# Performance work log

Hardware: AMD Instinct MI355X
Metric: run time of the kernel (lower is better)

The kernel has to match this reference:

```python
import jax, jax.numpy as jnp
import numpy as np

L = 2        # rnn_num_layer
H = 512      # rnn_hidden_size
E = 512      # embed_dim == rnn_input_size
B = 16
T_DEC = 512
S_ENC = 512
VOCAB = 1001 # num_embed
OUT = 1000   # output_size
PAD = 0.0


def setup_inputs() -> dict:
    key = jax.random.key(0)
    ks = jax.random.split(key, 16)
    s = 0.05
    trg_inputs = jax.random.randint(ks[0], (B, T_DEC), 0, VOCAB)
    trg_len = jnp.clip(jax.random.randint(ks[1], (B,), 0, T_DEC + 1), 1, T_DEC)
    encoder_outputs = jax.random.normal(ks[2], (B, S_ENC, H), dtype=jnp.float32)
    h0 = jax.random.normal(ks[3], (L * 2, B, H), dtype=jnp.float32)
    c0 = jax.random.normal(ks[4], (L * 2, B, H), dtype=jnp.float32)
    embed = jax.random.normal(ks[5], (VOCAB, E)) * s
    W_ih0 = jax.random.normal(ks[6], (2, 4 * H, E)) * s          # layer 0, fwd/bwd dirs
    W_ih1 = jax.random.normal(ks[7], (L - 1, 2, 4 * H, 2 * H)) * s  # layers>0 take concat(fwd,bwd)
    W_hh = jax.random.normal(ks[8], (L, 2, 4 * H, H)) * s
    b_ih = jax.random.normal(ks[9], (L, 2, 4 * H)) * s
    b_hh = jax.random.normal(ks[10], (L, 2, 4 * H)) * s
    W_att = jax.random.normal(ks[11], (H, H)) * s  # Attention 'general' linear
    b_att = jax.random.normal(ks[12], (H,)) * s
    W_fc = jax.random.normal(ks[13], (OUT, 2 * H)) * s
    b_fc = jax.random.normal(ks[14], (OUT,)) * s
    return dict(trg_inputs=trg_inputs, trg_len=trg_len, encoder_outputs=encoder_outputs,
                h0=h0, c0=c0, embed=embed, W_ih0=W_ih0, W_ih1=W_ih1, W_hh=W_hh,
                b_ih=b_ih, b_hh=b_hh, W_att=W_att, b_att=b_att, W_fc=W_fc, b_fc=b_fc)


def _cell(x, h, c, Wi, Wh, bi, bh):
    # PyTorch LSTM gate order: i, f, g, o
    g = x @ Wi.T + h @ Wh.T + bi + bh  # [B, 4H]
    i, f, gg, o = jnp.split(g, 4, axis=-1)
    c2 = jax.nn.sigmoid(f) * c + jax.nn.sigmoid(i) * jnp.tanh(gg)
    h2 = jax.nn.sigmoid(o) * jnp.tanh(c2)
    return h2, c2


def _decode(trg_inputs, trg_len, encoder_outputs, h0, c0, embed,
            W_ih0, W_ih1, W_hh, b_ih, b_hh, W_att, b_att, W_fc, b_fc):
    Bb, T = trg_inputs.shape
    S = encoder_outputs.shape[1]
    # 'general' attention projection of encoder outputs (hoisted out of the loop)
    enc_proj = jnp.einsum('bsh,gh->bsg', encoder_outputs, W_att) + b_att
    enc_mask = jnp.arange(S)[None, :] < trg_len[:, None]          # [B, S]
    step_valid = jnp.arange(T)[:, None] < trg_len[None, :]        # [T, B]
    h = h0.reshape(L, 2, Bb, H)
    c = c0.reshape(L, 2, Bb, H)

    def step(carry, xt):
        h, c = carry
        tok, valid = xt                                           # [B], [B]
        xin = embed[tok]                                          # [B, E]
        hs, cs = [], []
        for l in range(L):
            Wi = W_ih0 if l == 0 else W_ih1[l - 1]
            hf, cf = _cell(xin, h[l, 0], c[l, 0], Wi[0], W_hh[l, 0], b_ih[l, 0], b_hh[l, 0])
            hb, cb = _cell(xin, h[l, 1], c[l, 1], Wi[1], W_hh[l, 1], b_ih[l, 1], b_hh[l, 1])
            hs.append(jnp.stack([hf, hb]))
            cs.append(jnp.stack([cf, cb]))
            xin = jnp.concatenate([hf, hb], axis=-1)              # input to next layer [B, 2H]
        h2 = jnp.stack(hs)
        c2 = jnp.stack(cs)
        dec = hs[-1][0] + hs[-1][1]                               # sum fwd+bwd halves [B, H]
        score = jnp.einsum('bh,bsh->bs', dec, enc_proj)
        score = jnp.where(enc_mask, score, -1e30)                 # ragged length mask
        att = jax.nn.softmax(score, axis=-1)
        ctx = jnp.einsum('bs,bsh->bh', att, encoder_outputs)
        fc = jnp.concatenate([dec, ctx], axis=-1) @ W_fc.T + b_fc # [B, OUT]
        out = jnp.where(valid[:, None], fc, PAD)                  # positions past trg_len stay pad
        return (h2, c2), out

    _, outs = jax.lax.scan(step, (h, c), (trg_inputs.T, step_valid))
    return outs.transpose(1, 0, 2)                                # [B, T, OUT]


def reference(trg_inputs, trg_len, encoder_outputs, h0, c0, embed,
              W_ih0, W_ih1, W_hh, b_ih, b_hh, W_att, b_att, W_fc, b_fc):
    return _decode(trg_inputs, trg_len, encoder_outputs, h0, c0, embed,
                   W_ih0, W_ih1, W_hh, b_ih, b_hh, W_att, b_att, W_fc, b_fc)
```

## Files before the change

kernel.cpp:

```cpp
#include <hip/hip_runtime.h>
#include <cstdint>
#include <cstddef>

typedef __attribute__((ext_vector_type(8))) short short8;
typedef __attribute__((ext_vector_type(4))) float f32x4;
typedef __attribute__((ext_vector_type(4))) unsigned int uint4v;

#define DEV static __device__ __forceinline__

DEV float b2f(unsigned short u){ union{unsigned int i; float f;} v; v.i = ((unsigned int)u)<<16; return v.f; }
DEV unsigned short f2b(float f){
  union{float f; unsigned int i;} v; v.f = f;
  unsigned int u = v.i;
  unsigned int r = (u + 0x7fffu + ((u>>16)&1u)) >> 16;
  return (unsigned short)r;
}
DEV float sigm(float x){ return 1.0f/(1.0f + __expf(-x)); }
DEV float tanhfast(float x){ return 1.0f - 2.0f/(1.0f + __expf(2.0f*x)); }

DEV uint4v ld_sc_b128(const unsigned short* p){
  uint4v d;
  asm volatile("global_load_dwordx4 %0, %1, off sc0 sc1" : "=v"(d) : "v"(p) : "memory");
  return d;
}
DEV short8 ldw8(const float* p){
  short8 w;
  #pragma unroll
  for (int e = 0; e < 8; ++e) w[e] = (short)f2b(p[e]);
  return w;
}

__global__ __launch_bounds__(256) void k_cast(const float* __restrict__ s, unsigned short* __restrict__ d, int n){
  int i = blockIdx.x*256 + threadIdx.x;
  if (i < n) d[i] = f2b(s[i]);
}
__global__ __launch_bounds__(256) void k_transpose_enc(const float* __restrict__ enc, unsigned short* __restrict__ encT){
  int i = blockIdx.x*256 + threadIdx.x;
  if (i >= 16*512*512) return;
  int b = i >> 18, r = i & 262143, h = r >> 9, s = r & 511;
  encT[i] = f2b(enc[(b<<18) + (s<<9) + h]);
}
__global__ __launch_bounds__(256) void k_gather(const int* __restrict__ trg, const float* __restrict__ emb, unsigned short* __restrict__ X){
  int i = blockIdx.x*256 + threadIdx.x;
  if (i >= 8192*512) return;
  int r = i >> 9, e = i & 511;
  int t = r >> 4, b = r & 15;
  int tok = trg[(b<<9) + t];
  X[i] = f2b(emb[((size_t)tok<<9) + e]);
}
__global__ __launch_bounds__(256) void k_bsum(const float* __restrict__ bi, const float* __restrict__ bh, float* __restrict__ o){
  int i = blockIdx.x*256 + threadIdx.x;
  if (i < 8192) o[i] = bi[i] + bh[i];
}
__global__ __launch_bounds__(256) void k_init(const float* __restrict__ h0, unsigned short* __restrict__ Hst0,
                                              unsigned short* __restrict__ Hst1, unsigned int* __restrict__ bar){
  int i = blockIdx.x*256 + threadIdx.x;
  if (i < 256) bar[i] = 0;
  if (i < 16384) {
    Hst0[i] = f2b(h0[i]);
    Hst1[i] = f2b(h0[16384 + i]);
  }
}
__global__ __launch_bounds__(256) void k_split(const float* __restrict__ S, unsigned short* __restrict__ H,
                                               unsigned short* __restrict__ L, int n){
  int i = blockIdx.x*256 + threadIdx.x;
  if (i >= n) return;
  float f = S[i];
  unsigned short hi = f2b(f);
  H[i] = hi;
  L[i] = f2b(f - b2f(hi));
}
__global__ __launch_bounds__(256) void k_decsplit(const float* __restrict__ HF, unsigned short* __restrict__ DCTX,
                                                  unsigned short* __restrict__ DH, unsigned short* __restrict__ DL){
  int i = blockIdx.x*256 + threadIdx.x;
  if (i >= 8192*512) return;
  int r = i >> 9, j = i & 511;
  float d = HF[((size_t)r<<10) + j] + HF[((size_t)r<<10) + 512 + j];
  unsigned short hi = f2b(d);
  DCTX[((size_t)r<<10) + j] = hi;
  DH[i] = hi;
  DL[i] = f2b(d - b2f(hi));
}

template<int MODE>
__global__ __launch_bounds__(256) void k_gemm(
    const unsigned short* __restrict__ A, long lda, long sA,
    const unsigned short* __restrict__ W, long ldw, long sW,
    void* __restrict__ C, long ldc, long sC,
    const float* __restrict__ bias,
    int M, int N, int K,
    const int* __restrict__ tlen)
{
  __shared__ short8 AsV[128*5];
  __shared__ short8 WsV[128*5];
  const int bz = blockIdx.z;
  const unsigned short* Ab = A + (size_t)bz * sA;
  const unsigned short* Wb = W + (size_t)bz * sW;
  const int m0 = blockIdx.x << 7, n0 = blockIdx.y << 7;
  const int tid = threadIdx.x;
  const int wave = tid >> 6, lane = tid & 63;
  const int ln = lane & 15, kq = lane >> 4;
  const int wm = wave >> 1, wn = wave & 1;
  const int ar0 = tid >> 2, ac0 = (tid & 3) << 3;
  const int ar1 = ar0 + 64;
  const short8 z8 = {0,0,0,0,0,0,0,0};

  f32x4 acc[4][4];
  #pragma unroll
  for (int i = 0; i < 4; ++i)
    #pragma unroll
    for (int j = 0; j < 4; ++j) { f32x4 z = {0.f,0.f,0.f,0.f}; acc[i][j] = z; }

  for (int k0 = 0; k0 < K; k0 += 32) {
    short8 a0 = *(const short8*)(Ab + (size_t)(m0+ar0)*lda + k0 + ac0);
    short8 a1 = *(const short8*)(Ab + (size_t)(m0+ar1)*lda + k0 + ac0);
    short8 w0 = z8, w1 = z8;
    if (MODE != 2 || (n0+ar0) < N) w0 = *(const short8*)(Wb + (size_t)(n0+ar0)*ldw + k0 + ac0);
    if (MODE != 2 || (n0+ar1) < N) w1 = *(const short8*)(Wb + (size_t)(n0+ar1)*ldw + k0 + ac0);
    __syncthreads();
    AsV[ar0*5 + (ac0>>3)] = a0;
    AsV[ar1*5 + (ac0>>3)] = a1;
    WsV[ar0*5 + (ac0>>3)] = w0;
    WsV[ar1*5 + (ac0>>3)] = w1;
    __syncthreads();
    short8 af[4], wf[4];
    #pragma unroll
    for (int i = 0; i < 4; ++i) af[i] = AsV[((wm<<6) + (i<<4) + ln)*5 + kq];
    #pragma unroll
    for (int i = 0; i < 4; ++i) wf[i] = WsV[((wn<<6) + (i<<4) + ln)*5 + kq];
    #pragma unroll
    for (int i = 0; i < 4; ++i)
      #pragma unroll
      for (int j = 0; j < 4; ++j)
        acc[i][j] = __builtin_amdgcn_mfma_f32_16x16x32_bf16(af[i], wf[j], acc[i][j], 0, 0, 0);
  }
  #pragma unroll
  for (int j = 0; j < 4; ++j) {
    const int n = n0 + (wn<<6) + (j<<4) + ln;
    float bi = 0.f;
    if (MODE == 0 || MODE == 1) { if (bias) bi = bias[n]; }
    if (MODE == 2) { if (n < N) bi = bias[n]; }
    #pragma unroll
    for (int i = 0; i < 4; ++i) {
      #pragma unroll
      for (int r = 0; r < 4; ++r) {
        const int m = m0 + (wm<<6) + (i<<4) + (kq<<2) + r;
        float v = acc[i][j][r] + bi;
        if (MODE == 0) ((unsigned short*)C)[(size_t)bz*sC + (size_t)m*ldc + n] = f2b(v);
        else if (MODE == 1) ((float*)C)[(size_t)bz*sC + (size_t)m*ldc + n] = v;
        else if (MODE == 3) ((float*)C)[(size_t)bz*sC + (size_t)m*ldc + n] += v;
        else {
          if (n < N) {
            int tt = m >> 4, bb = m & 15;
            ((float*)C)[((size_t)((bb<<9) + tt))*1000 + n] = (tt < tlen[bb]) ? v : 0.0f;
          }
        }
      }
    }
  }
}

__global__ __launch_bounds__(256, 1) void k_recur(
    const float* __restrict__ whh,
    const float* __restrict__ wih1,
    const unsigned short* __restrict__ Xg0,
    const float* __restrict__ c0all,
    const float* __restrict__ bsum,
    unsigned short* __restrict__ Hst0,
    unsigned short* __restrict__ Hst1,
    unsigned short* __restrict__ Hcat,
    float* __restrict__ HcatF,
    unsigned int* __restrict__ flags)
{
  const int bid = blockIdx.x;
  const int dir = (bid >> 5) & 1;
  const int j0  = (bid & 31) << 4;
  const int tid = threadIdx.x;
  const int wave = tid >> 6, lane = tid & 63;
  const int ln = lane & 15, kq = lane >> 4;
  const int b_ = tid >> 4, jl = tid & 15;
  const int myfl = bid & 31, pollfl = lane & 31;

  __shared__ __align__(16) unsigned char h0sh[32768];
  __shared__ __align__(16) unsigned char h1sh[16384];
  __shared__ float gsh[4][16][16];

  unsigned int* FL0d0 = flags;
  unsigned int* FL0d1 = flags + 32;

  if (bid < 64) {
    unsigned int* FL = flags + (dir << 5);
    short8 wfrag[16];
    {
      const float* wb = whh + (((size_t)((dir<<11) + (wave<<9) + j0 + ln)) << 9) + (kq<<3);
      #pragma unroll
      for (int ks = 0; ks < 16; ++ks) wfrag[ks] = ldw8(wb + (ks<<5));
    }
    float c = c0all[(((size_t)((dir<<4) + b_)) << 9) + j0 + jl];

    size_t xr = ((size_t)b_ << 12) + (dir<<11) + j0 + jl;
    float xg0 = b2f(Xg0[xr]);
    float xg1 = b2f(Xg0[xr + 512]);
    float xg2 = b2f(Xg0[xr + 1024]);
    float xg3 = b2f(Xg0[xr + 1536]);

    for (int t = 0; t < 512; ++t) {
      const unsigned short* hbase = Hst0 + ((((t&1)<<1) + dir)<<13);
      uint4v st[4];
      #pragma unroll
      for (int cc = 0; cc < 4; ++cc)
        st[cc] = ld_sc_b128(hbase + (cc<<11) + (tid<<3));
      asm volatile("s_waitcnt vmcnt(0)" ::: "memory");
      #pragma unroll
      for (int cc = 0; cc < 4; ++cc) {
        int g = (cc<<8) + tid, row = g >> 6, slot = g & 63, ps = slot ^ row;
        *(uint4v*)(h1sh + row*1024 + (ps<<4)) = st[cc];
      }
      __syncthreads();

      f32x4 acc0 = {0.f,0.f,0.f,0.f}, acc1 = {0.f,0.f,0.f,0.f};
      #pragma unroll
      for (int ks = 0; ks < 16; ks += 2) {
        short8 a0 = *(const short8*)(h1sh + ln*1024 + ((((ks<<2)+kq) ^ ln)<<4));
        short8 a1 = *(const short8*)(h1sh + ln*1024 + (((((ks+1)<<2)+kq) ^ ln)<<4));
        acc0 = __builtin_amdgcn_mfma_f32_16x16x32_bf16(a0, wfrag[ks],   acc0, 0, 0, 0);
        acc1 = __builtin_amdgcn_mfma_f32_16x16x32_bf16(a1, wfrag[ks+1], acc1, 0, 0, 0);
      }
      f32x4 acc = acc0 + acc1;
      #pragma unroll
      for (int r = 0; r < 4; ++r)
        gsh[wave][(kq<<2)+r][ln] = acc[r];
      __syncthreads();

      float gi = gsh[0][b_][jl] + xg0;
      float gf = gsh[1][b_][jl] + xg1;
      float gg = gsh[2][b_][jl] + xg2;
      float go = gsh[3][b_][jl] + xg3;
      float ii = sigm(gi), ff = sigm(gf);
      float g2 = tanhfast(gg), oo = sigm(go);
      c = ff*c + ii*g2;
      float h = oo * tanhfast(c);
      unsigned short h16 = f2b(h);

      unsigned int hu = (unsigned int)h16;
      unsigned int hv1 = __shfl_down(hu, 1);
      unsigned int hv2 = __shfl_down(hu, 2);
      unsigned int hv3 = __shfl_down(hu, 3);
      if (!(lane & 3)) {
        unsigned long long hq = (unsigned long long)(hu | (hv1 << 16))
                              | ((unsigned long long)(hv2 | (hv3 << 16)) << 32);
        unsigned short* dst = Hst0 + (((((t+1)&1)<<1) + dir)<<13) + (b_<<9) + j0 + jl;
        __hip_atomic_store((unsigned long long*)dst, hq, __ATOMIC_RELAXED, __HIP_MEMORY_SCOPE_AGENT);
        unsigned short* dc = Hcat + (((size_t)((t<<4) + b_))<<10) + (dir<<9) + j0 + jl;
        __hip_atomic_store((unsigned long long*)dc, hq, __ATOMIC_RELAXED, __HIP_MEMORY_SCOPE_AGENT);
      }

      if (t < 511) {
        xr = (((size_t)(((t+1)<<4) + b_)) << 12) + (dir<<11) + j0 + jl;
        xg0 = b2f(Xg0[xr]);
        xg1 = b2f(Xg0[xr + 512]);
        xg2 = b2f(Xg0[xr + 1024]);
        xg3 = b2f(Xg0[xr + 1536]);
      }

      __syncthreads();
      if (tid == 0)
        __hip_atomic_store(FL + myfl, (unsigned int)(t + 1), __ATOMIC_RELAXED, __HIP_MEMORY_SCOPE_AGENT);
      if (t == 511) break;

      if (wave == 0) {
        const unsigned int tgt = (unsigned int)(t + 1);
        while (!__all((int)(__hip_atomic_load(FL + pollfl, __ATOMIC_RELAXED, __HIP_MEMORY_SCOPE_AGENT) >= tgt)))
          __builtin_amdgcn_s_sleep(1);
      }
      __syncthreads();
    }
  } else {
    unsigned int* FL = flags + 64 + (dir << 5);
    short8 whf[16];
    {
      const float* wb = whh + 2097152 + (((size_t)((dir<<11) + (wave<<9) + j0 + ln)) << 9) + (kq<<3);
      #pragma unroll
      for (int ks = 0; ks < 16; ++ks) whf[ks] = ldw8(wb + (ks<<5));
    }
    short8 wxf[32];
    {
      const float* xb = wih1 + (((size_t)((dir<<11) + (wave<<9) + j0 + ln)) << 10) + (kq<<3);
      #pragma unroll
      for (int ks = 0; ks < 32; ++ks) wxf[ks] = ldw8(xb + (ks<<5));
    }
    float c = c0all[16384 + (((size_t)((dir<<4) + b_)) << 9) + j0 + jl];
    float bs0 = bsum[4096 + (dir<<11) + 0*512 + j0 + jl];
    float bs1 = bsum[4096 + (dir<<11) + 1*512 + j0 + jl];
    float bs2 = bsum[4096 + (dir<<11) + 2*512 + j0 + jl];
    float bs3 = bsum[4096 + (dir<<11) + 3*512 + j0 + jl];

    if (wave == 0) {
      const unsigned int* fp = (lane < 32) ? (FL0d0 + lane) : (FL0d1 + (lane - 32));
      while (!__all((int)(__hip_atomic_load(fp, __ATOMIC_RELAXED, __HIP_MEMORY_SCOPE_AGENT) >= 2u)))
        __builtin_amdgcn_s_sleep(1);
    }
    __syncthreads();

    uint4v sxr[8];
    #pragma unroll
    for (int cc = 0; cc < 8; ++cc) {
      int g = (cc<<8) + tid, row = g >> 7, slot = g & 127;
      sxr[cc] = ld_sc_b128(Hcat + (row<<10) + (slot<<3));
    }

    for (int t = 0; t < 512; ++t) {
      asm volatile("s_waitcnt vmcnt(0)" ::: "memory");
      #pragma unroll
      for (int cc = 0; cc < 8; ++cc) {
        int g = (cc<<8) + tid, row = g >> 7, slot = g & 127, ps = slot ^ row;
        *(uint4v*)(h0sh + row*2048 + (ps<<4)) = sxr[cc];
      }
      const unsigned short* h1base = Hst1 + ((((t&1)<<1) + dir)<<13);
      uint4v sh[4];
      #pragma unroll
      for (int cc = 0; cc < 4; ++cc)
        sh[cc] = ld_sc_b128(h1base + (cc<<11) + (tid<<3));
      asm volatile("s_waitcnt vmcnt(0)" ::: "memory");
      #pragma unroll
      for (int cc = 0; cc < 4; ++cc) {
        int g = (cc<<8) + tid, row = g >> 6, slot = g & 63, ps = slot ^ row;
        *(uint4v*)(h1sh + row*1024 + (ps<<4)) = sh[cc];
      }
      __syncthreads();

      f32x4 acc0 = {0.f,0.f,0.f,0.f}, acc1 = {0.f,0.f,0.f,0.f};
      #pragma unroll
      for (int ks = 0; ks < 32; ks += 2) {
        short8 a0 = *(const short8*)(h0sh + ln*2048 + ((((ks<<2)+kq) ^ ln)<<4));
        short8 a1 = *(const short8*)(h0sh + ln*2048 + (((((ks+1)<<2)+kq) ^ ln)<<4));
        acc0 = __builtin_amdgcn_mfma_f32_16x16x32_bf16(a0, wxf[ks],   acc0, 0, 0, 0);
        acc1 = __builtin_amdgcn_mfma_f32_16x16x32_bf16(a1, wxf[ks+1], acc1, 0, 0, 0);
      }
      #pragma unroll
      for (int ks = 0; ks < 16; ks += 2) {
        short8 a0 = *(const short8*)(h1sh + ln*1024 + ((((ks<<2)+kq) ^ ln)<<4));
        short8 a1 = *(const short8*)(h1sh + ln*1024 + (((((ks+1)<<2)+kq) ^ ln)<<4));
        acc0 = __builtin_amdgcn_mfma_f32_16x16x32_bf16(a0, whf[ks],   acc0, 0, 0, 0);
        acc1 = __builtin_amdgcn_mfma_f32_16x16x32_bf16(a1, whf[ks+1], acc1, 0, 0, 0);
      }
      f32x4 acc = acc0 + acc1;
      #pragma unroll
      for (int r = 0; r < 4; ++r)
        gsh[wave][(kq<<2)+r][ln] = acc[r];
      __syncthreads();

      float gi = gsh[0][b_][jl] + bs0;
      float gf = gsh[1][b_][jl] + bs1;
      float gg = gsh[2][b_][jl] + bs2;
      float go = gsh[3][b_][jl] + bs3;
      float ii = sigm(gi), ff = sigm(gf);
      float g2 = tanhfast(gg), oo = sigm(go);
      c = ff*c + ii*g2;
      float h = oo * tanhfast(c);
      unsigned short h16 = f2b(h);

      unsigned int hu = (unsigned int)h16;
      unsigned int hv1 = __shfl_down(hu, 1);
      unsigned int hv2 = __shfl_down(hu, 2);
      unsigned int hv3 = __shfl_down(hu, 3);
      if (!(lane & 3)) {
        unsigned long long hq = (unsigned long long)(hu | (hv1 << 16))
                              | ((unsigned long long)(hv2 | (hv3 << 16)) << 32);
        unsigned short* dst = Hst1 + (((((t+1)&1)<<1) + dir)<<13) + (b_<<9) + j0 + jl;
        __hip_atomic_store((unsigned long long*)dst, hq, __ATOMIC_RELAXED, __HIP_MEMORY_SCOPE_AGENT);
      }

      __syncthreads();
      if (tid == 0)
        __hip_atomic_store(FL + myfl, (unsigned int)(t + 1), __ATOMIC_RELAXED, __HIP_MEMORY_SCOPE_AGENT);

      __builtin_nontemporal_store(h, HcatF + (((size_t)((t<<4) + b_))<<10) + (dir<<9) + j0 + jl);

      if (t < 511) {
        const unsigned short* hb0 = Hcat + (((size_t)(t+1)) << 14);
        #pragma unroll
        for (int cc = 0; cc < 8; ++cc) {
          int g = (cc<<8) + tid, row = g >> 7, slot = g & 127;
          sxr[cc] = ld_sc_b128(hb0 + (row<<10) + (slot<<3));
        }
      }

      if (t == 511) break;

      if (wave == 0) {
        const unsigned int tgt = (unsigned int)(t + 1);
        while (!__all((int)(__hip_atomic_load(FL + pollfl, __ATOMIC_RELAXED, __HIP_MEMORY_SCOPE_AGENT) >= tgt)))
          __builtin_amdgcn_s_sleep(1);
      } else if (wave == 1) {
        const unsigned int tgt = (t + 3 < 512) ? (unsigned int)(t + 3) : 512u;
        const unsigned int* fp = (lane < 32) ? (FL0d0 + lane) : (FL0d1 + (lane - 32));
        while (!__all((int)(__hip_atomic_load(fp, __ATOMIC_RELAXED, __HIP_MEMORY_SCOPE_AGENT) >= tgt)))
          __builtin_amdgcn_s_sleep(1);
      }
      __syncthreads();
    }
  }
}

__global__ __launch_bounds__(256) void k_softmax(const float* __restrict__ score, const int* __restrict__ tlen,
                                                 unsigned short* __restrict__ att){
  int row = (blockIdx.x<<2) + (threadIdx.x>>6);
  int lane = threadIdx.x & 63;
  int b = row >> 9;
  int len = tlen[b];
  const float* sr = score + ((size_t)row<<9);
  float v[8]; float m = -3.0e38f;
  #pragma unroll
  for (int i = 0; i < 8; ++i) {
    int s = (i<<6) + lane;
    float x = sr[s];
    v[i] = (s < len) ? x : -1.0e30f;
    m = fmaxf(m, v[i]);
  }
  #pragma unroll
  for (int off = 32; off; off >>= 1) m = fmaxf(m, __shfl_xor(m, off));
  float sum = 0.f; float p[8];
  #pragma unroll
  for (int i = 0; i < 8; ++i) { p[i] = __expf(v[i] - m); sum += p[i]; }
  #pragma unroll
  for (int off = 32; off; off >>= 1) sum += __shfl_xor(sum, off);
  float inv = 1.0f / sum;
  unsigned short* ar = att + ((size_t)row<<9);
  #pragma unroll
  for (int i = 0; i < 8; ++i) ar[(i<<6) + lane] = f2b(p[i]*inv);
}

extern "C" void kernel_launch(void* const* d_in, const int* in_sizes, int n_in,
                              void* d_out, int out_size, void* d_ws, size_t ws_size,
                              hipStream_t stream) {
  (void)in_sizes; (void)n_in; (void)out_size; (void)ws_size;
  const int*   trg  = (const int*)d_in[0];
  const int*   tlen = (const int*)d_in[1];
  const float* enc  = (const float*)d_in[2];
  const float* h0   = (const float*)d_in[3];
  const float* c0   = (const float*)d_in[4];
  const float* emb  = (const float*)d_in[5];
  const float* wih0 = (const float*)d_in[6];
  const float* wih1 = (const float*)d_in[7];
  const float* whh  = (const float*)d_in[8];
  const float* bih  = (const float*)d_in[9];
  const float* bhh  = (const float*)d_in[10];
  const float* watt = (const float*)d_in[11];
  const float* batt = (const float*)d_in[12];
  const float* wfc  = (const float*)d_in[13];
  const float* bfc  = (const float*)d_in[14];
  float* out = (float*)d_out;

  char* ws = (char*)d_ws;
  size_t off = 0;
  auto alloc = [&](size_t bytes)->char* {
    char* p = ws + off; off += (bytes + 255) & ~(size_t)255; return p;
  };
  unsigned int*   BAR   = (unsigned int*)  alloc(1024);
  unsigned short* XEMB  = (unsigned short*)alloc(8192ll*512*2);
  unsigned short* WI0B  = (unsigned short*)alloc(4096ll*512*2);
  unsigned short* WFCB  = (unsigned short*)alloc(1000ll*1024*2);
  unsigned short* WATTB = (unsigned short*)alloc(512ll*512*2);
  unsigned short* ENCB  = (unsigned short*)alloc(8192ll*512*2);
  unsigned short* ENCT  = (unsigned short*)alloc(8192ll*512*2);
  float*          BSUM  = (float*)         alloc(8192*4);
  unsigned short* HST0  = (unsigned short*)alloc(32768*2);
  unsigned short* HST1  = (unsigned short*)alloc(32768*2);
  unsigned short* XG    = (unsigned short*)alloc(8192ll*4096*2);
  unsigned short* HCAT  = (unsigned short*)alloc(8192ll*1024*2);
  float*          HCATF = (float*)         alloc(8192ll*1024*4);
  float*          SCORE = (float*)         alloc(8192ll*512*4);
  unsigned short* ENCPH = (unsigned short*)alloc(8192ll*512*2);
  unsigned short* ENCPL = (unsigned short*)alloc(8192ll*512*2);
  unsigned short* DECH  = (unsigned short*)alloc(8192ll*512*2);
  unsigned short* DECL  = (unsigned short*)alloc(8192ll*512*2);
  unsigned short* ATT   = (unsigned short*)alloc(8192ll*512*2);
  unsigned short* DCTX  = (unsigned short*)alloc(8192ll*1024*2);

  auto cdiv = [](long a, long b){ return (int)((a + b - 1) / b); };

  k_cast<<<cdiv(2097152,256),256,0,stream>>>(wih0, WI0B, 2097152);
  k_cast<<<cdiv(1024000,256),256,0,stream>>>(wfc,  WFCB, 1024000);
  k_cast<<<cdiv(262144,256),256,0,stream>>>(watt, WATTB, 262144);
  k_cast<<<cdiv(4194304,256),256,0,stream>>>(enc,  ENCB, 4194304);
  k_transpose_enc<<<cdiv(4194304,256),256,0,stream>>>(enc, ENCT);
  k_gather<<<cdiv(4194304,256),256,0,stream>>>(trg, emb, XEMB);
  k_bsum<<<cdiv(8192,256),256,0,stream>>>(bih, bhh, BSUM);
  k_init<<<cdiv(32768,256),256,0,stream>>>(h0, HST0, HST1, BAR);

  k_gemm<1><<<dim3(64,4,1),256,0,stream>>>(ENCB,512,0, WATTB,512,0, (void*)SCORE,512,0, batt, 8192,512,512, nullptr);
  k_split<<<cdiv(4194304,256),256,0,stream>>>(SCORE, ENCPH, ENCPL, 4194304);

  k_gemm<0><<<dim3(64,32,1),256,0,stream>>>(XEMB,512,0, WI0B,512,0, (void*)XG,4096,0, BSUM, 8192,4096,512, nullptr);

  k_recur<<<128,256,0,stream>>>(whh, wih1, XG, c0, BSUM, HST0, HST1, HCAT, HCATF, BAR);

  k_decsplit<<<cdiv(4194304,256),256,0,stream>>>(HCATF, DCTX, DECH, DECL);

  k_gemm<1><<<dim3(4,4,16),256,0,stream>>>(DECH,8192,512, ENCPH,512,262144, (void*)SCORE,512,262144, nullptr, 512,512,512, nullptr);
  k_gemm<3><<<dim3(4,4,16),256,0,stream>>>(DECH,8192,512, ENCPL,512,262144, (void*)SCORE,512,262144, nullptr, 512,512,512, nullptr);
  k_gemm<3><<<dim3(4,4,16),256,0,stream>>>(DECL,8192,512, ENCPH,512,262144, (void*)SCORE,512,262144, nullptr, 512,512,512, nullptr);

  k_softmax<<<2048,256,0,stream>>>(SCORE, tlen, ATT);

  k_gemm<0><<<dim3(4,4,16),256,0,stream>>>(ATT,512,262144, ENCT,512,262144, (void*)(DCTX+512),16384,1024, nullptr, 512,512,512, nullptr);

  k_gemm<2><<<dim3(64,8,1),256,0,stream>>>(DCTX,1024,0, WFCB,1024,0, (void*)out,1000,0, bfc, 8192,1000,1024, tlen);
}
```

Baseline: 2.110 ms.

## Precompute next-step layer-1 input GEMM early and merge split-bf16 score GEMMs

In the recurrent kernel, the layer-1 input-projection MFMA over the layer-0 hidden state is computed for step t+1 at the end of step t, and prefetch runs two steps ahead. Each step's critical path after the flag wait then holds only the recurrent-weight MFMAs. Separately, the three hi/lo bf16 score GEMMs (hi*hi, hi*lo, lo*hi) become one GEMM with K=1536 over concatenated [hi,lo,hi] and [hi,hi,lo] operands, reusing the XG buffer. This removes two launches and the read-modify-write accumulation. The flag-wait ordering changes to make the producer data ready before the early compute, which risks subtle synchronization errors.

```diff
diff --git a/kernel.cpp b/kernel.cpp
--- a/kernel.cpp
+++ b/kernel.cpp
@@ -61,25 +61,31 @@
     Hst1[i] = f2b(h0[16384 + i]);
   }
 }
-__global__ __launch_bounds__(256) void k_split(const float* __restrict__ S, unsigned short* __restrict__ H,
-                                               unsigned short* __restrict__ L, int n){
+__global__ __launch_bounds__(256) void k_split(const float* __restrict__ S, unsigned short* __restrict__ E3, int n){
   int i = blockIdx.x*256 + threadIdx.x;
   if (i >= n) return;
+  int r = i >> 9, j = i & 511;
   float f = S[i];
   unsigned short hi = f2b(f);
-  H[i] = hi;
-  L[i] = f2b(f - b2f(hi));
+  unsigned short lo = f2b(f - b2f(hi));
+  size_t base = (size_t)r * 1536 + j;
+  E3[base] = hi;
+  E3[base + 512] = lo;
+  E3[base + 1024] = hi;
 }
 __global__ __launch_bounds__(256) void k_decsplit(const float* __restrict__ HF, unsigned short* __restrict__ DCTX,
-                                                  unsigned short* __restrict__ DH, unsigned short* __restrict__ DL){
+                                                  unsigned short* __restrict__ D3){
   int i = blockIdx.x*256 + threadIdx.x;
   if (i >= 8192*512) return;
   int r = i >> 9, j = i & 511;
   float d = HF[((size_t)r<<10) + j] + HF[((size_t)r<<10) + 512 + j];
   unsigned short hi = f2b(d);
+  unsigned short lo = f2b(d - b2f(hi));
   DCTX[((size_t)r<<10) + j] = hi;
-  DH[i] = hi;
-  DL[i] = f2b(d - b2f(hi));
+  size_t base = (size_t)r * 1536 + j;
+  D3[base] = hi;
+  D3[base + 512] = hi;
+  D3[base + 1024] = lo;
 }
 
 template<int MODE>
@@ -148,7 +154,6 @@
         float v = acc[i][j][r] + bi;
         if (MODE == 0) ((unsigned short*)C)[(size_t)bz*sC + (size_t)m*ldc + n] = f2b(v);
         else if (MODE == 1) ((float*)C)[(size_t)bz*sC + (size_t)m*ldc + n] = v;
-        else if (MODE == 3) ((float*)C)[(size_t)bz*sC + (size_t)m*ldc + n] += v;
         else {
           if (n < N) {
             int tt = m >> 4, bb = m & 15;
@@ -308,14 +313,45 @@
       int g = (cc<<8) + tid, row = g >> 7, slot = g & 127;
       sxr[cc] = ld_sc_b128(Hcat + (row<<10) + (slot<<3));
     }
+    asm volatile("s_waitcnt vmcnt(0)" ::: "memory");
+    #pragma unroll
+    for (int cc = 0; cc < 8; ++cc) {
+      int g = (cc<<8) + tid, row = g >> 7, slot = g & 127, ps = slot ^ row;
+      *(uint4v*)(h0sh + row*2048 + (ps<<4)) = sxr[cc];
+    }
+    __syncthreads();
+    f32x4 xacc;
+    {
+      f32x4 xa = {0.f,0.f,0.f,0.f}, xb2 = {0.f,0.f,0.f,0.f};
+      #pragma unroll
+      for (int ks = 0; ks < 32; ks += 2) {
+        short8 a0 = *(const short8*)(h0sh + ln*2048 + ((((ks<<2)+kq) ^ ln)<<4));
+        short8 a1 = *(const short8*)(h0sh + ln*2048 + (((((ks+1)<<2)+kq) ^ ln)<<4));
+        xa  = __builtin_amdgcn_mfma_f32_16x16x32_bf16(a0, wxf[ks],   xa, 0, 0, 0);
+        xb2 = __builtin_amdgcn_mfma_f32_16x16x32_bf16(a1, wxf[ks+1], xb2, 0, 0, 0);
+      }
+      xacc = xa + xb2;
+    }
+    #pragma unroll
+    for (int cc = 0; cc < 8; ++cc) {
+      int g = (cc<<8) + tid, row = g >> 7, slot = g & 127;
+      sxr[cc] = ld_sc_b128(Hcat + 16384 + (row<<10) + (slot<<3));
+    }
 
     for (int t = 0; t < 512; ++t) {
-      asm volatile("s_waitcnt vmcnt(0)" ::: "memory");
-      #pragma unroll
-      for (int cc = 0; cc < 8; ++cc) {
-        int g = (cc<<8) + tid, row = g >> 7, slot = g & 127, ps = slot ^ row;
-        *(uint4v*)(h0sh + row*2048 + (ps<<4)) = sxr[cc];
-      }
+      if (wave == 0) {
+        const unsigned int tgt = (unsigned int)t;
+        if (t > 0)
+          while (!__all((int)(__hip_atomic_load(FL + pollfl, __ATOMIC_RELAXED, __HIP_MEMORY_SCOPE_AGENT) >= tgt)))
+            __builtin_amdgcn_s_sleep(1);
+      } else if (wave == 1) {
+        const unsigned int tgt = (t + 3 < 512) ? (unsigned int)(t + 3) : 512u;
+        const unsigned int* fp = (lane < 32) ? (FL0d0 + lane) : (FL0d1 + (lane - 32));
+        while (!__all((int)(__hip_atomic_load(fp, __ATOMIC_RELAXED, __HIP_MEMORY_SCOPE_AGENT) >= tgt)))
+          __builtin_amdgcn_s_sleep(1);
+      }
+      __syncthreads();
+
       const unsigned short* h1base = Hst1 + ((((t&1)<<1) + dir)<<13);
       uint4v sh[4];
       #pragma unroll
@@ -329,14 +365,7 @@
       }
       __syncthreads();
 
-      f32x4 acc0 = {0.f,0.f,0.f,0.f}, acc1 = {0.f,0.f,0.f,0.f};
-      #pragma unroll
-      for (int ks = 0; ks < 32; ks += 2) {
-        short8 a0 = *(const short8*)(h0sh + ln*2048 + ((((ks<<2)+kq) ^ ln)<<4));
-        short8 a1 = *(const short8*)(h0sh + ln*2048 + (((((ks+1)<<2)+kq) ^ ln)<<4));
-        acc0 = __builtin_amdgcn_mfma_f32_16x16x32_bf16(a0, wxf[ks],   acc0, 0, 0, 0);
-        acc1 = __builtin_amdgcn_mfma_f32_16x16x32_bf16(a1, wxf[ks+1], acc1, 0, 0, 0);
-      }
+      f32x4 acc0 = xacc, acc1 = {0.f,0.f,0.f,0.f};
       #pragma unroll
       for (int ks = 0; ks < 16; ks += 2) {
         short8 a0 = *(const short8*)(h1sh + ln*1024 + ((((ks<<2)+kq) ^ ln)<<4));
@@ -377,28 +406,33 @@
 
       __builtin_nontemporal_store(h, HcatF + (((size_t)((t<<4) + b_))<<10) + (dir<<9) + j0 + jl);
 
-      if (t < 511) {
-        const unsigned short* hb0 = Hcat + (((size_t)(t+1)) << 14);
+      if (t == 511) break;
+
+      #pragma unroll
+      for (int cc = 0; cc < 8; ++cc) {
+        int g = (cc<<8) + tid, row = g >> 7, slot = g & 127, ps = slot ^ row;
+        *(uint4v*)(h0sh + row*2048 + (ps<<4)) = sxr[cc];
+      }
+      __syncthreads();
+      {
+        f32x4 xa = {0.f,0.f,0.f,0.f}, xb2 = {0.f,0.f,0.f,0.f};
+        #pragma unroll
+        for (int ks = 0; ks < 32; ks += 2) {
+          short8 a0 = *(const short8*)(h0sh + ln*2048 + ((((ks<<2)+kq) ^ ln)<<4));
+          short8 a1 = *(const short8*)(h0sh + ln*2048 + (((((ks+1)<<2)+kq) ^ ln)<<4));
+          xa  = __builtin_amdgcn_mfma_f32_16x16x32_bf16(a0, wxf[ks],   xa, 0, 0, 0);
+          xb2 = __builtin_amdgcn_mfma_f32_16x16x32_bf16(a1, wxf[ks+1], xb2, 0, 0, 0);
+        }
+        xacc = xa + xb2;
+      }
+      if (t < 510) {
+        const unsigned short* hb0 = Hcat + (((size_t)(t+2)) << 14);
         #pragma unroll
         for (int cc = 0; cc < 8; ++cc) {
           int g = (cc<<8) + tid, row = g >> 7, slot = g & 127;
           sxr[cc] = ld_sc_b128(hb0 + (row<<10) + (slot<<3));
         }
       }
-
-      if (t == 511) break;
-
-      if (wave == 0) {
-        const unsigned int tgt = (unsigned int)(t + 1);
-        while (!__all((int)(__hip_atomic_load(FL + pollfl, __ATOMIC_RELAXED, __HIP_MEMORY_SCOPE_AGENT) >= tgt)))
-          __builtin_amdgcn_s_sleep(1);
-      } else if (wave == 1) {
-        const unsigned int tgt = (t + 3 < 512) ? (unsigned int)(t + 3) : 512u;
-        const unsigned int* fp = (lane < 32) ? (FL0d0 + lane) : (FL0d1 + (lane - 32));
-        while (!__all((int)(__hip_atomic_load(fp, __ATOMIC_RELAXED, __HIP_MEMORY_SCOPE_AGENT) >= tgt)))
-          __builtin_amdgcn_s_sleep(1);
-      }
-      __syncthreads();
     }
   }
 }
@@ -471,12 +505,10 @@
   unsigned short* HCAT  = (unsigned short*)alloc(8192ll*1024*2);
   float*          HCATF = (float*)         alloc(8192ll*1024*4);
   float*          SCORE = (float*)         alloc(8192ll*512*4);
-  unsigned short* ENCPH = (unsigned short*)alloc(8192ll*512*2);
-  unsigned short* ENCPL = (unsigned short*)alloc(8192ll*512*2);
-  unsigned short* DECH  = (unsigned short*)alloc(8192ll*512*2);
-  unsigned short* DECL  = (unsigned short*)alloc(8192ll*512*2);
   unsigned short* ATT   = (unsigned short*)alloc(8192ll*512*2);
   unsigned short* DCTX  = (unsigned short*)alloc(8192ll*1024*2);
+  unsigned short* DEC3  = XG;
+  unsigned short* ENC3  = XG + 8192ll*1536;
 
   auto cdiv = [](long a, long b){ return (int)((a + b - 1) / b); };
 
@@ -490,17 +522,15 @@
   k_init<<<cdiv(32768,256),256,0,stream>>>(h0, HST0, HST1, BAR);
 
   k_gemm<1><<<dim3(64,4,1),256,0,stream>>>(ENCB,512,0, WATTB,512,0, (void*)SCORE,512,0, batt, 8192,512,512, nullptr);
-  k_split<<<cdiv(4194304,256),256,0,stream>>>(SCORE, ENCPH, ENCPL, 4194304);
 
   k_gemm<0><<<dim3(64,32,1),256,0,stream>>>(XEMB,512,0, WI0B,512,0, (void*)XG,4096,0, BSUM, 8192,4096,512, nullptr);
 
   k_recur<<<128,256,0,stream>>>(whh, wih1, XG, c0, BSUM, HST0, HST1, HCAT, HCATF, BAR);
 
-  k_decsplit<<<cdiv(4194304,256),256,0,stream>>>(HCATF, DCTX, DECH, DECL);
-
-  k_gemm<1><<<dim3(4,4,16),256,0,stream>>>(DECH,8192,512, ENCPH,512,262144, (void*)SCORE,512,262144, nullptr, 512,512,512, nullptr);
-  k_gemm<3><<<dim3(4,4,16),256,0,stream>>>(DECH,8192,512, ENCPL,512,262144, (void*)SCORE,512,262144, nullptr, 512,512,512, nullptr);
-  k_gemm<3><<<dim3(4,4,16),256,0,stream>>>(DECL,8192,512, ENCPH,512,262144, (void*)SCORE,512,262144, nullptr, 512,512,512, nullptr);
+  k_split<<<cdiv(4194304,256),256,0,stream>>>(SCORE, ENC3, 4194304);
+  k_decsplit<<<cdiv(4194304,256),256,0,stream>>>(HCATF, DCTX, DEC3);
+
+  k_gemm<1><<<dim3(4,4,16),256,0,stream>>>(DEC3,24576,1536, ENC3,1536,786432, (void*)SCORE,512,262144, nullptr, 512,512,1536, nullptr);
 
   k_softmax<<<2048,256,0,stream>>>(SCORE, tlen, ATT);
 
```

After: 1.846 ms, median of 2. -12.5%, faster.
